# Optimization experiments

Measured on AMD Instinct MI355X. Metric: run time of the kernel, lower is better.

## Reference

```python
import jax, jax.numpy as jnp
import numpy as np

B, S, V, T = 4096, 200, 33, 50  # batch, seq_len, num_var, len(time_range)
SURV_VAL, LONG_VAL = 1.0, 1.0
EPS = 1e-08


def setup_inputs() -> dict:
    key = jax.random.key(0)
    k1, k2, k3, k4, k5, k6 = jax.random.split(key, 6)
    long_pred = jax.random.normal(k1, (B, S, V - 1), dtype=jnp.float32)
    data = jax.random.normal(k2, (B, S, V), dtype=jnp.float32)
    # each row has a valid prefix of length in [2, S]; the rest is NaN padding
    lengths = jax.random.randint(k3, (B,), 2, S + 1)
    nanmask = jnp.arange(S)[None, :] >= lengths[:, None]  # [B, S]
    data = jnp.where(nanmask[:, :, None], jnp.nan, data)
    surv_pred = jax.random.uniform(k4, (B, T), dtype=jnp.float32)
    surv_pred = surv_pred / surv_pred.sum(axis=1, keepdims=True)  # P(T=t|x) rows
    event = jax.random.randint(k5, (B,), 0, 2).astype(bool)
    event_time = jax.random.uniform(k6, (B,), dtype=jnp.float32) * (T - 1.0)
    time_range = jnp.arange(T, dtype=jnp.float32)
    return {"long_pred": long_pred, "surv_pred": surv_pred, "data": data,
            "event": event, "event_time": event_time, "time_range": time_range}


def _nll(surv_pred, event, event_time_idx):
    # f[i] = pred[i, idx]           if event
    #      = sum_{j > idx} pred[i,j] otherwise  (suffix sum via reversed cumsum)
    rc = jnp.cumsum(surv_pred[:, ::-1], axis=1)[:, ::-1]  # rc[:,k] = sum_{j>=k}
    at_idx = jnp.take_along_axis(surv_pred, event_time_idx[:, None], axis=1)[:, 0]
    idxp1 = jnp.clip(event_time_idx + 1, 0, T - 1)
    tail = jnp.where(event_time_idx + 1 < T,
                     jnp.take_along_axis(rc, idxp1[:, None], axis=1)[:, 0], 0.0)
    f = jnp.where(event, at_idx, tail)
    f = jnp.where(f == 0.0, EPS, f)
    return -jnp.mean(jnp.log(f))


def _long_loss(long_pred, data):
    x = data[:, :, 1:]                       # [B, S, V-1]
    valid = ~jnp.isnan(x[:, :, 0])           # [B, S] history mask
    idx_last = valid.sum(axis=1) - 1         # last valid visit per row
    histmask = valid & (jnp.arange(S)[None, :] != idx_last[:, None])
    # pair prediction at t with data at t+1 (futuremask = histmask shifted right)
    m = histmask[:, :-1]                     # [B, S-1]
    diff = jnp.where(m[:, :, None], long_pred[:, :-1, :] - x[:, 1:, :], 0.0)
    denom = m.sum().astype(jnp.float32) * (V - 1)
    return jnp.sum(diff * diff) / denom


def reference(long_pred, surv_pred, data, event, event_time, time_range):
    event_time_idx = jnp.searchsorted(time_range, event_time, side='right') - 1
    nll = _nll(surv_pred, event, event_time_idx)
    ll = _long_loss(long_pred, data)
    return SURV_VAL * nll + LONG_VAL * ll
```

## Files before the change

kernel.cpp:

```cpp
#include <hip/hip_runtime.h>
#include <cstdint>
#include <cstddef>

#define B 4096
#define S 200
#define V 33
#define T 50
#define EPSV 1e-08

#define NLLB 1024
#define GRID (NLLB + B)


using f4  = __attribute__((ext_vector_type(4))) float;
using f4u = __attribute__((aligned(4))) f4;

__device__ __forceinline__ bool is_nan_bits(float x) {
    uint32_t u = __float_as_uint(x);
    return (u & 0x7F800000u) == 0x7F800000u && (u & 0x007FFFFFu) != 0u;
}

template <int D>
__device__ __forceinline__ void sweep_batch(const float* __restrict__ lpbase,
                                            const float* __restrict__ dbase,
                                            int k0, int nvec,
                                            float& acc, int& cnt) {
    f4 lpv[D], dv[D];
    #pragma unroll
    for (int u = 0; u < D; ++u) {
        int k  = k0 + u * 256;
        int kc = k < nvec ? k : (nvec - 1);
        int j  = kc * 4;
        int sr = kc >> 3;
        lpv[u] = *reinterpret_cast<const f4*>(lpbase + j);
        dv[u]  = *reinterpret_cast<const f4u*>(dbase + j + sr + 34);
    }
    #pragma unroll
    for (int u = 0; u < D; ++u) {
        int k = k0 + u * 256;
        if (k < nvec) {
            #pragma unroll
            for (int i = 0; i < 4; ++i) {
                float de = dv[u][i];
                float df = lpv[u][i] - de;
                if (is_nan_bits(de)) df = 0.0f;
                acc = fmaf(df, df, acc);
            }
            if ((k & 7) == 0 && !is_nan_bits(dv[u][0])) cnt++;
        }
    }
}

__global__ __launch_bounds__(256, 4)
void fused_kernel(const float* __restrict__ long_pred,
                  const float* __restrict__ surv_pred,
                  const float* __restrict__ data,
                  const uint32_t* __restrict__ event_words,
                  const float* __restrict__ event_time,
                  const float* __restrict__ time_range,
                  double* __restrict__ ll_part,
                  int* __restrict__ lenm1,
                  double* __restrict__ nll_part) {
    const int tid  = threadIdx.x;
    const int blk  = blockIdx.x;
    const int wib  = tid >> 6;
    const int lane = tid & 63;

    if (blk < NLLB) {
        __shared__ int s_gt1, s_oddnz;
        if (tid == 0) { s_gt1 = 0; s_oddnz = 0; }
        __syncthreads();
        int gt1 = 0, oddnz = 0;
        for (int i = tid; i < B / 4; i += 256) {
            uint32_t w = event_words[i];
            if (w > 1u) gt1 = 1;
            if ((i & 1) && w != 0u) oddnz = 1;
        }
        if (gt1)   atomicOr(&s_gt1, 1);
        if (oddnz) atomicOr(&s_oddnz, 1);
        __syncthreads();
        const int mode = s_gt1 ? 1 : (s_oddnz ? 0 : 2);

        const int b = blk * 4 + wib;
        float sv = (lane < T) ? surv_pred[b * T + lane] : 0.0f;
        float tr = (lane < T) ? time_range[lane] : 0.0f;
        float et = event_time[b];

        unsigned long long bal = __ballot(lane < T && tr <= et);
        int idx = (int)__popcll(bal) - 1;

        float tval = (lane < T && lane >= idx + 1) ? sv : 0.0f;
        for (int off = 32; off > 0; off >>= 1) tval += __shfl_down(tval, off);

        int   idx_c  = idx < 0 ? 0 : idx;
        float at_idx = __shfl(sv, idx_c);

        bool ev;
        if (mode == 1)      ev = ((const unsigned char*)event_words)[b] != 0;
        else if (mode == 2) ev = ((const int*)event_words)[2 * b] != 0;
        else                ev = ((const int*)event_words)[b] != 0;

        __shared__ double s_n[4];
        if (lane == 0) {
            float f = ev ? at_idx : ((idx + 1 < T) ? tval : 0.0f);
            if (f == 0.0f) f = (float)EPSV;
            s_n[wib] = -(double)logf(f);
        }
        __syncthreads();
        if (tid == 0) nll_part[blk] = s_n[0] + s_n[1] + s_n[2] + s_n[3];
    } else {
        const int b = blk - NLLB;
        const float* __restrict__ dbase  = data      + (size_t)b * (S * V);
        const float* __restrict__ lpbase = long_pred + (size_t)b * (S * (V - 1));

        int valid = 0;
        if (tid < 50) valid = !is_nan_bits(dbase[(size_t)(4 * tid + 3) * V + 1]);
        const int c1 = __syncthreads_count(valid);
        const int bound_rows = min(4 * c1 + 2, S - 1);
        const int nvec = bound_rows * 8;

        float acc = 0.0f;
        int   cnt = 0;
        sweep_batch<4>(lpbase, dbase, tid, nvec, acc, cnt);
        if (nvec > 1024)
            sweep_batch<3>(lpbase, dbase, tid + 1024, nvec, acc, cnt);

        for (int off = 32; off > 0; off >>= 1) {
            acc += __shfl_down(acc, off);
            cnt += __shfl_down(cnt, off);
        }
        __shared__ float s_red[4];
        __shared__ int   s_cnt[4];
        if (lane == 0) { s_red[wib] = acc; s_cnt[wib] = cnt; }
        __syncthreads();
        if (tid == 0) {
            ll_part[b] = (double)s_red[0] + (double)s_red[1]
                       + (double)s_red[2] + (double)s_red[3];
            lenm1[b]   = s_cnt[0] + s_cnt[1] + s_cnt[2] + s_cnt[3];
        }
    }
}

__global__ __launch_bounds__(256)
void finalize_kernel(const double* __restrict__ ll_part,
                     const int* __restrict__ lenm1,
                     const double* __restrict__ nll_part,
                     float* __restrict__ out) {
    const int tid = threadIdx.x;
    double ls = 0.0, ns = 0.0;
    long long cs = 0;
    for (int i = tid; i < B; i += 256)    { ls += ll_part[i]; cs += lenm1[i]; }
    for (int i = tid; i < NLLB; i += 256) ns += nll_part[i];

    for (int off = 32; off > 0; off >>= 1) {
        ls += __shfl_down(ls, off);
        ns += __shfl_down(ns, off);
        cs += __shfl_down(cs, off);
    }
    __shared__ double    sl[4], sn[4];
    __shared__ long long sc[4];
    const int wib = tid >> 6, lane = tid & 63;
    if (lane == 0) { sl[wib] = ls; sn[wib] = ns; sc[wib] = cs; }
    __syncthreads();
    if (tid == 0) {
        double L = 0.0, N = 0.0;
        long long C = 0;
        for (int i = 0; i < 4; ++i) { L += sl[i]; N += sn[i]; C += sc[i]; }
        double denom = (double)C * (double)(V - 1);
        out[0] = (float)(N / (double)B + L / denom);
    }
}

extern "C" void kernel_launch(void* const* d_in, const int* in_sizes, int n_in,
                              void* d_out, int out_size, void* d_ws, size_t ws_size,
                              hipStream_t stream) {
    const float* long_pred  = (const float*)d_in[0];
    const float* surv_pred  = (const float*)d_in[1];
    const float* data       = (const float*)d_in[2];
    const void*  event      = d_in[3];
    const float* event_time = (const float*)d_in[4];
    const float* time_range = (const float*)d_in[5];
    float* out = (float*)d_out;

    double* ll_part  = (double*)d_ws;
    int*    lenm1    = (int*)((char*)d_ws + 32768);
    double* nll_part = (double*)((char*)d_ws + 49152);

    fused_kernel<<<GRID, 256, 0, stream>>>(
        long_pred, surv_pred, data, (const uint32_t*)event, event_time,
        time_range, ll_part, lenm1, nll_part);
    finalize_kernel<<<1, 256, 0, stream>>>(ll_part, lenm1, nll_part, out);
}
```

Before: 31.30 us.

## Prefetch first row loads before NaN-bound sync and batch NLL blocks

The long-loss blocks now issue their first 512 vector loads before the __syncthreads_count that computes the valid-row bound, so memory latency overlaps the bound computation. The remaining loads are split into guarded 512 and 768 stages. NLL work moves to 128 trailing blocks that each handle 32 rows, instead of 1024 leading blocks with 4 rows each, which cuts block-launch overhead and the redundant event-word scans. This trades less parallelism on the NLL side for loads that may be wasted on rows with short valid prefixes.

```diff
diff --git a/kernel.cpp b/kernel.cpp
--- a/kernel.cpp
+++ b/kernel.cpp
@@ -8,8 +8,8 @@
 #define T 50
 #define EPSV 1e-08
 
-#define NLLB 1024
-#define GRID (NLLB + B)
+#define NLLB 128
+#define GRID (B + NLLB)
 
 
 using f4  = __attribute__((ext_vector_type(4))) float;
@@ -20,25 +20,28 @@
     return (u & 0x7F800000u) == 0x7F800000u && (u & 0x007FFFFFu) != 0u;
 }
 
-template <int D>
-__device__ __forceinline__ void sweep_batch(const float* __restrict__ lpbase,
+template <int D, bool CLAMP>
+__device__ __forceinline__ void issue_loads(const float* __restrict__ lpbase,
                                             const float* __restrict__ dbase,
-                                            int k0, int nvec,
-                                            float& acc, int& cnt) {
-    f4 lpv[D], dv[D];
+                                            int k0, int nvec, f4* lpv, f4* dv) {
     #pragma unroll
     for (int u = 0; u < D; ++u) {
         int k  = k0 + u * 256;
-        int kc = k < nvec ? k : (nvec - 1);
+        int kc = CLAMP ? (k < nvec ? k : nvec - 1) : k;
         int j  = kc * 4;
         int sr = kc >> 3;
         lpv[u] = *reinterpret_cast<const f4*>(lpbase + j);
         dv[u]  = *reinterpret_cast<const f4u*>(dbase + j + sr + 34);
     }
+}
+
+template <int D, bool GUARD>
+__device__ __forceinline__ void accum(const f4* lpv, const f4* dv,
+                                      int k0, int nvec, float& acc, int& cnt) {
     #pragma unroll
     for (int u = 0; u < D; ++u) {
         int k = k0 + u * 256;
-        if (k < nvec) {
+        if (!GUARD || k < nvec) {
             #pragma unroll
             for (int i = 0; i < 4; ++i) {
                 float de = dv[u][i];
@@ -66,7 +69,51 @@
     const int wib  = tid >> 6;
     const int lane = tid & 63;
 
-    if (blk < NLLB) {
+    if (blk < B) {
+        const int b = blk;
+        const float* __restrict__ dbase  = data      + (size_t)b * (S * V);
+        const float* __restrict__ lpbase = long_pred + (size_t)b * (S * (V - 1));
+
+        f4 lp1[2], d1[2];
+        issue_loads<2, false>(lpbase, dbase, tid, 0, lp1, d1);
+
+        int valid = 0;
+        if (tid < 50) valid = !is_nan_bits(dbase[(size_t)(4 * tid + 3) * V + 1]);
+        const int c1 = __syncthreads_count(valid);
+        const int bound_rows = min(4 * c1 + 2, S - 1);
+        const int nvec = bound_rows * 8;
+
+        float acc = 0.0f;
+        int   cnt = 0;
+        accum<2, false>(lp1, d1, tid, 0, acc, cnt);
+
+        if (nvec > 512) {
+            f4 lp2[2], d2[2];
+            issue_loads<2, true>(lpbase, dbase, tid + 512, nvec, lp2, d2);
+            accum<2, true>(lp2, d2, tid + 512, nvec, acc, cnt);
+        }
+        if (nvec > 1024) {
+            f4 lp3[3], d3[3];
+            issue_loads<3, true>(lpbase, dbase, tid + 1024, nvec, lp3, d3);
+            accum<3, true>(lp3, d3, tid + 1024, nvec, acc, cnt);
+        }
+
+        for (int off = 32; off > 0; off >>= 1) {
+            acc += __shfl_down(acc, off);
+            cnt += __shfl_down(cnt, off);
+        }
+        __shared__ float s_red[4];
+        __shared__ int   s_cnt[4];
+        if (lane == 0) { s_red[wib] = acc; s_cnt[wib] = cnt; }
+        __syncthreads();
+        if (tid == 0) {
+            ll_part[b] = (double)s_red[0] + (double)s_red[1]
+                       + (double)s_red[2] + (double)s_red[3];
+            lenm1[b]   = s_cnt[0] + s_cnt[1] + s_cnt[2] + s_cnt[3];
+        }
+    } else {
+        const int nb = blk - B;
+
         __shared__ int s_gt1, s_oddnz;
         if (tid == 0) { s_gt1 = 0; s_oddnz = 0; }
         __syncthreads();
@@ -81,63 +128,39 @@
         __syncthreads();
         const int mode = s_gt1 ? 1 : (s_oddnz ? 0 : 2);
 
-        const int b = blk * 4 + wib;
-        float sv = (lane < T) ? surv_pred[b * T + lane] : 0.0f;
-        float tr = (lane < T) ? time_range[lane] : 0.0f;
-        float et = event_time[b];
-
-        unsigned long long bal = __ballot(lane < T && tr <= et);
-        int idx = (int)__popcll(bal) - 1;
-
-        float tval = (lane < T && lane >= idx + 1) ? sv : 0.0f;
-        for (int off = 32; off > 0; off >>= 1) tval += __shfl_down(tval, off);
-
-        int   idx_c  = idx < 0 ? 0 : idx;
-        float at_idx = __shfl(sv, idx_c);
-
-        bool ev;
-        if (mode == 1)      ev = ((const unsigned char*)event_words)[b] != 0;
-        else if (mode == 2) ev = ((const int*)event_words)[2 * b] != 0;
-        else                ev = ((const int*)event_words)[b] != 0;
+        double nsum = 0.0;
+        #pragma unroll
+        for (int r = 0; r < 8; ++r) {
+            const int b = nb * 32 + r * 4 + wib;
+            float sv = (lane < T) ? surv_pred[b * T + lane] : 0.0f;
+            float tr = (lane < T) ? time_range[lane] : 0.0f;
+            float et = event_time[b];
+
+            unsigned long long bal = __ballot(lane < T && tr <= et);
+            int idx = (int)__popcll(bal) - 1;
+
+            float tval = (lane < T && lane >= idx + 1) ? sv : 0.0f;
+            for (int off = 32; off > 0; off >>= 1) tval += __shfl_down(tval, off);
+
+            int   idx_c  = idx < 0 ? 0 : idx;
+            float at_idx = __shfl(sv, idx_c);
+
+            bool ev;
+            if (mode == 1)      ev = ((const unsigned char*)event_words)[b] != 0;
+            else if (mode == 2) ev = ((const int*)event_words)[2 * b] != 0;
+            else                ev = ((const int*)event_words)[b] != 0;
+
+            if (lane == 0) {
+                float f = ev ? at_idx : ((idx + 1 < T) ? tval : 0.0f);
+                if (f == 0.0f) f = (float)EPSV;
+                nsum += -(double)logf(f);
+            }
+        }
 
         __shared__ double s_n[4];
-        if (lane == 0) {
-            float f = ev ? at_idx : ((idx + 1 < T) ? tval : 0.0f);
-            if (f == 0.0f) f = (float)EPSV;
-            s_n[wib] = -(double)logf(f);
-        }
-        __syncthreads();
-        if (tid == 0) nll_part[blk] = s_n[0] + s_n[1] + s_n[2] + s_n[3];
-    } else {
-        const int b = blk - NLLB;
-        const float* __restrict__ dbase  = data      + (size_t)b * (S * V);
-        const float* __restrict__ lpbase = long_pred + (size_t)b * (S * (V - 1));
-
-        int valid = 0;
-        if (tid < 50) valid = !is_nan_bits(dbase[(size_t)(4 * tid + 3) * V + 1]);
-        const int c1 = __syncthreads_count(valid);
-        const int bound_rows = min(4 * c1 + 2, S - 1);
-        const int nvec = bound_rows * 8;
-
-        float acc = 0.0f;
-        int   cnt = 0;
-        sweep_batch<4>(lpbase, dbase, tid, nvec, acc, cnt);
-        if (nvec > 1024)
-            sweep_batch<3>(lpbase, dbase, tid + 1024, nvec, acc, cnt);
-
-        for (int off = 32; off > 0; off >>= 1) {
-            acc += __shfl_down(acc, off);
-            cnt += __shfl_down(cnt, off);
-        }
-        __shared__ float s_red[4];
-        __shared__ int   s_cnt[4];
-        if (lane == 0) { s_red[wib] = acc; s_cnt[wib] = cnt; }
-        __syncthreads();
-        if (tid == 0) {
-            ll_part[b] = (double)s_red[0] + (double)s_red[1]
-                       + (double)s_red[2] + (double)s_red[3];
-            lenm1[b]   = s_cnt[0] + s_cnt[1] + s_cnt[2] + s_cnt[3];
-        }
+        if (lane == 0) s_n[wib] = nsum;
+        __syncthreads();
+        if (tid == 0) nll_part[nb] = s_n[0] + s_n[1] + s_n[2] + s_n[3];
     }
 }
 
@@ -150,7 +173,7 @@
     double ls = 0.0, ns = 0.0;
     long long cs = 0;
     for (int i = tid; i < B; i += 256)    { ls += ll_part[i]; cs += lenm1[i]; }
-    for (int i = tid; i < NLLB; i += 256) ns += nll_part[i];
+    if (tid < NLLB) ns = nll_part[tid];
 
     for (int off = 32; off > 0; off >>= 1) {
         ls += __shfl_down(ls, off);
```

Result: slower. 36.16 us (+15.5%).
